# Kernel tuning notes

Hardware: AMD Instinct MI355X
Metric: run time of the kernel (lower is better)

Reference implementation:

```python
import jax, jax.numpy as jnp
import numpy as np
from itertools import permutations

M = 10          # number of masked tokens (logits.size(0) when whole_word=False)
VOCAB = 50257   # n_class


def setup_inputs() -> dict:
    key = jax.random.key(0)
    k1, k2 = jax.random.split(key)
    logits = jax.random.normal(k1, (M, VOCAB), dtype=jnp.float32)
    target = jax.random.randint(k2, (M,), 0, VOCAB, dtype=jnp.int64).astype(jnp.int32)
    # All M! permutations, enumerated exactly as itertools.permutations (lexicographic),
    # matching the torch module's iteration order (ties broken by first strict improvement).
    perms = jnp.asarray(np.array(list(permutations(range(M))), dtype=np.int32))
    return {"logits": logits, "target": target, "perms": perms}


def reference(logits, target, perms):
    # prob[i, v] = softmax over classes
    prob = jax.nn.softmax(logits, axis=-1)                      # [M, V]
    # S[i, j] = prob[i, target[j]]  (score of assigning slot j's target to position i)
    S = prob[:, target]                                         # [M, M]
    # score(p) = sum_i prob[i, target[p[i]]] = sum_i S[i, p[i]]
    rows = jnp.arange(S.shape[0], dtype=jnp.int32)[None, :]     # [1, M]
    scores = S[rows, perms].sum(axis=-1)                        # [P]
    # torch loop keeps the FIRST permutation achieving the max (strict > update);
    # jnp.argmax also returns the first occurrence of the max.
    best = jnp.argmax(scores)
    target_best = target[perms[best]]                           # [M]
    # CrossEntropyLoss(reduction='none') == -log_softmax gathered at target
    logp = jax.nn.log_softmax(logits, axis=-1)                  # [M, V]
    loss = -jnp.take_along_axis(logp, target_best[:, None].astype(jnp.int32), axis=1)[:, 0]
    return loss, target_best
```

## Files before the change

kernel.cpp:

```cpp
#include <hip/hip_runtime.h>

#define VOCAB 50257
#define M 10
#define NPERM 3628800
#define CHUNKS 32
#define CH 1571
#define NTHREADS_PERM 151200
#define PERM_BLOCKS 591

#define WS_PMAX 0
#define WS_PSUM 320
#define WS_RMAX 640
#define WS_RSUM 656
#define WS_S    672

__global__ __launch_bounds__(256) void chunkstats_kernel(
    const float* __restrict__ logits, float* __restrict__ ws) {
    const int r = blockIdx.x >> 5;
    const int c = blockIdx.x & 31;
    const int s = c * CH;
    const int e = (s + CH < VOCAB) ? s + CH : VOCAB;
    const float* __restrict__ x = logits + (size_t)r * VOCAB;
    const int tid = threadIdx.x;
    __shared__ float wred[4];

    float m = -3.4e38f;
    for (int j = s + tid; j < e; j += 256) m = fmaxf(m, x[j]);
    #pragma unroll
    for (int off = 32; off; off >>= 1) m = fmaxf(m, __shfl_down(m, off, 64));
    if ((tid & 63) == 0) wred[tid >> 6] = m;
    __syncthreads();
    const float cm = fmaxf(fmaxf(wred[0], wred[1]), fmaxf(wred[2], wred[3]));
    __syncthreads();

    float sum = 0.f;
    for (int j = s + tid; j < e; j += 256) sum += expf(x[j] - cm);
    #pragma unroll
    for (int off = 32; off; off >>= 1) sum += __shfl_down(sum, off, 64);
    if ((tid & 63) == 0) wred[tid >> 6] = sum;
    __syncthreads();
    if (tid == 0) {
        ws[WS_PMAX + blockIdx.x] = cm;
        ws[WS_PSUM + blockIdx.x] = wred[0] + wred[1] + wred[2] + wred[3];
    }
}

__global__ __launch_bounds__(320) void combine_kernel(
    const float* __restrict__ logits, const int* __restrict__ target,
    float* __restrict__ ws) {
    const int tid = threadIdx.x;
    const int r = tid >> 5;
    const float lm = ws[WS_PMAX + tid];
    float m = lm;
    #pragma unroll
    for (int off = 16; off; off >>= 1) m = fmaxf(m, __shfl_xor(m, off, 32));
    float contrib = ws[WS_PSUM + tid] * expf(lm - m);
    #pragma unroll
    for (int off = 16; off; off >>= 1) contrib += __shfl_xor(contrib, off, 32);
    if ((tid & 31) == 0) {
        ws[WS_RMAX + r] = m;
        ws[WS_RSUM + r] = contrib;
    }
    __syncthreads();
    if (tid < 100) {
        const int i = tid / 10;
        const int k = tid % 10;
        const int t = target[k];
        ws[WS_S + tid] =
            expf(logits[(size_t)i * VOCAB + t] - ws[WS_RMAX + i]) / ws[WS_RSUM + i];
    }
}

__global__ __launch_bounds__(256) void perm_kernel(
    const float* __restrict__ ws, unsigned long long* __restrict__ keys) {
    __shared__ float S[100];
    const int tid = threadIdx.x;
    if (tid < 100) S[tid] = ws[WS_S + tid];
    __syncthreads();

    const unsigned int t = blockIdx.x * 256u + tid;
    unsigned long long key = 0ull;
    if (t < NTHREADS_PERM) {
        const unsigned int base = t * 24u;
        unsigned int p = base;
        unsigned long long avail = 0x9876543210ull;
        float prefix = 0.f;
        const unsigned int fact6[6] = {362880u, 40320u, 5040u, 720u, 120u, 24u};
        #pragma unroll
        for (int pos = 0; pos < 6; ++pos) {
            const unsigned int f = fact6[pos];
            const unsigned int d = p / f;
            p -= d * f;
            const unsigned int sh = d * 4u;
            const unsigned int sym = (unsigned int)(avail >> sh) & 0xFu;
            avail = (avail & ((1ull << sh) - 1ull)) | ((avail >> (sh + 4u)) << sh);
            prefix += S[pos * 10 + sym];
        }
        const int q0 = (int)(avail & 0xF),        q1 = (int)((avail >> 4) & 0xF);
        const int q2 = (int)((avail >> 8) & 0xF), q3 = (int)((avail >> 12) & 0xF);
        const float s6[4] = {S[60+q0], S[60+q1], S[60+q2], S[60+q3]};
        const float s7[4] = {S[70+q0], S[70+q1], S[70+q2], S[70+q3]};
        const float s8[4] = {S[80+q0], S[80+q1], S[80+q2], S[80+q3]};
        const float s9[4] = {S[90+q0], S[90+q1], S[90+q2], S[90+q3]};
        constexpr unsigned char P[24][4] = {
            {0,1,2,3},{0,1,3,2},{0,2,1,3},{0,2,3,1},{0,3,1,2},{0,3,2,1},
            {1,0,2,3},{1,0,3,2},{1,2,0,3},{1,2,3,0},{1,3,0,2},{1,3,2,0},
            {2,0,1,3},{2,0,3,1},{2,1,0,3},{2,1,3,0},{2,3,0,1},{2,3,1,0},
            {3,0,1,2},{3,0,2,1},{3,1,0,2},{3,1,2,0},{3,2,0,1},{3,2,1,0}};
        float best = -1.f; unsigned int bl = 0;
        #pragma unroll
        for (int l = 0; l < 24; ++l) {
            const float sc =
                (((prefix + s6[P[l][0]]) + s7[P[l][1]]) + s8[P[l][2]]) + s9[P[l][3]];
            if (sc > best) { best = sc; bl = (unsigned int)l; }
        }
        const unsigned int gidx = base + bl;
        key = ((unsigned long long)__float_as_uint(best) << 32) |
              (unsigned long long)(0xFFFFFFFFu - gidx);
    }
    #pragma unroll
    for (int off = 32; off; off >>= 1) {
        const unsigned long long o = __shfl_down(key, off, 64);
        if (o > key) key = o;
    }
    __shared__ unsigned long long wk[4];
    if ((tid & 63) == 0) wk[tid >> 6] = key;
    __syncthreads();
    if (tid == 0) {
        unsigned long long k = wk[0];
        #pragma unroll
        for (int w = 1; w < 4; ++w) if (wk[w] > k) k = wk[w];
        keys[blockIdx.x] = k;
    }
}

__global__ __launch_bounds__(256) void final_kernel(
    const float* __restrict__ logits, const int* __restrict__ target,
    const float* __restrict__ ws, const unsigned long long* __restrict__ keys,
    float* __restrict__ out) {
    const int tid = threadIdx.x;
    unsigned long long k = 0ull;
    for (int i = tid; i < PERM_BLOCKS; i += 256) {
        const unsigned long long v = keys[i];
        if (v > k) k = v;
    }
    #pragma unroll
    for (int off = 32; off; off >>= 1) {
        const unsigned long long o = __shfl_down(k, off, 64);
        if (o > k) k = o;
    }
    __shared__ unsigned long long wk[4];
    __shared__ int perm[10];
    if ((tid & 63) == 0) wk[tid >> 6] = k;
    __syncthreads();
    if (tid == 0) {
        unsigned long long kk = wk[0];
        #pragma unroll
        for (int w = 1; w < 4; ++w) if (wk[w] > kk) kk = wk[w];
        unsigned int p = 0xFFFFFFFFu - (unsigned int)(kk & 0xFFFFFFFFull);
        unsigned long long avail = 0x9876543210ull;
        const unsigned int fact[9] = {362880u, 40320u, 5040u, 720u, 120u, 24u, 6u, 2u, 1u};
        #pragma unroll
        for (int pos = 0; pos < 9; ++pos) {
            const unsigned int f = fact[pos];
            const unsigned int d = p / f;
            p -= d * f;
            const unsigned int sh = d * 4u;
            perm[pos] = (int)((avail >> sh) & 0xFull);
            avail = (avail & ((1ull << sh) - 1ull)) | ((avail >> (sh + 4u)) << sh);
        }
        perm[9] = (int)(avail & 0xFull);
    }
    __syncthreads();
    if (tid < 10) {
        const int tb = target[perm[tid]];
        const float logp =
            logits[(size_t)tid * VOCAB + tb] - ws[WS_RMAX + tid] - logf(ws[WS_RSUM + tid]);
        out[tid]      = -logp;
        out[10 + tid] = (float)tb;
    }
}

extern "C" void kernel_launch(void* const* d_in, const int* in_sizes, int n_in,
                              void* d_out, int out_size, void* d_ws, size_t ws_size,
                              hipStream_t stream) {
    const float* logits = (const float*)d_in[0];
    const int*   target = (const int*)d_in[1];
    float* ws = (float*)d_ws;
    unsigned long long* keys = (unsigned long long*)((char*)d_ws + 4096);
    float* out = (float*)d_out;

    chunkstats_kernel<<<10 * CHUNKS, 256, 0, stream>>>(logits, ws);
    combine_kernel<<<1, 320, 0, stream>>>(logits, target, ws);
    perm_kernel<<<PERM_BLOCKS, 256, 0, stream>>>(ws, keys);
    final_kernel<<<1, 256, 0, stream>>>(logits, target, ws, keys, out);
}
```

Measured before the change: 18.20 us.

## Fuse combine, permutation search and final reduction into one last-block kernel

```diff
diff --git a/kernel.cpp b/kernel.cpp
--- a/kernel.cpp
+++ b/kernel.cpp
@@ -3,21 +3,20 @@
 #define VOCAB 50257
 #define M 10
 #define NPERM 3628800
-#define CHUNKS 32
-#define CH 1571
+#define CHUNKS 16
+#define CH 3142
 #define NTHREADS_PERM 151200
 #define PERM_BLOCKS 591
 
 #define WS_PMAX 0
-#define WS_PSUM 320
-#define WS_RMAX 640
-#define WS_RSUM 656
-#define WS_S    672
+#define WS_PSUM 160
 
 __global__ __launch_bounds__(256) void chunkstats_kernel(
-    const float* __restrict__ logits, float* __restrict__ ws) {
-    const int r = blockIdx.x >> 5;
-    const int c = blockIdx.x & 31;
+    const float* __restrict__ logits, float* __restrict__ ws,
+    unsigned int* __restrict__ counter) {
+    if (blockIdx.x == 0 && threadIdx.x == 0) *counter = 0u;
+    const int r = blockIdx.x >> 4;
+    const int c = blockIdx.x & 15;
     const int s = c * CH;
     const int e = (s + CH < VOCAB) ? s + CH : VOCAB;
     const float* __restrict__ x = logits + (size_t)r * VOCAB;
@@ -45,37 +44,31 @@
     }
 }
 
-__global__ __launch_bounds__(320) void combine_kernel(
+__global__ __launch_bounds__(256) void fused_perm_kernel(
     const float* __restrict__ logits, const int* __restrict__ target,
-    float* __restrict__ ws) {
+    const float* __restrict__ ws, unsigned long long* __restrict__ keys,
+    unsigned int* __restrict__ counter, float* __restrict__ out) {
+    __shared__ float S[100], rowmax[10], rowsum[10];
+    __shared__ unsigned long long wk[4];
+    __shared__ int perm[10];
+    __shared__ int isLast;
     const int tid = threadIdx.x;
-    const int r = tid >> 5;
-    const float lm = ws[WS_PMAX + tid];
-    float m = lm;
-    #pragma unroll
-    for (int off = 16; off; off >>= 1) m = fmaxf(m, __shfl_xor(m, off, 32));
-    float contrib = ws[WS_PSUM + tid] * expf(lm - m);
-    #pragma unroll
-    for (int off = 16; off; off >>= 1) contrib += __shfl_xor(contrib, off, 32);
-    if ((tid & 31) == 0) {
-        ws[WS_RMAX + r] = m;
-        ws[WS_RSUM + r] = contrib;
+
+    if (tid < 160) {
+        const float lm = ws[WS_PMAX + tid];
+        float m = lm;
+        #pragma unroll
+        for (int off = 8; off; off >>= 1) m = fmaxf(m, __shfl_xor(m, off, 16));
+        float c = ws[WS_PSUM + tid] * expf(lm - m);
+        #pragma unroll
+        for (int off = 8; off; off >>= 1) c += __shfl_xor(c, off, 16);
+        if ((tid & 15) == 0) { rowmax[tid >> 4] = m; rowsum[tid >> 4] = c; }
     }
     __syncthreads();
     if (tid < 100) {
-        const int i = tid / 10;
-        const int k = tid % 10;
-        const int t = target[k];
-        ws[WS_S + tid] =
-            expf(logits[(size_t)i * VOCAB + t] - ws[WS_RMAX + i]) / ws[WS_RSUM + i];
+        const int i = tid / 10, k = tid % 10;
+        S[tid] = expf(logits[(size_t)i * VOCAB + target[k]] - rowmax[i]) / rowsum[i];
     }
-}
-
-__global__ __launch_bounds__(256) void perm_kernel(
-    const float* __restrict__ ws, unsigned long long* __restrict__ keys) {
-    __shared__ float S[100];
-    const int tid = threadIdx.x;
-    if (tid < 100) S[tid] = ws[WS_S + tid];
     __syncthreads();
 
     const unsigned int t = blockIdx.x * 256u + tid;
@@ -123,7 +116,6 @@
         const unsigned long long o = __shfl_down(key, off, 64);
         if (o > key) key = o;
     }
-    __shared__ unsigned long long wk[4];
     if ((tid & 63) == 0) wk[tid >> 6] = key;
     __syncthreads();
     if (tid == 0) {
@@ -131,14 +123,14 @@
         #pragma unroll
         for (int w = 1; w < 4; ++w) if (wk[w] > k) k = wk[w];
         keys[blockIdx.x] = k;
+        __threadfence();
+        const unsigned int prev = atomicAdd(counter, 1u);
+        isLast = (prev == PERM_BLOCKS - 1) ? 1 : 0;
     }
-}
+    __syncthreads();
+    if (!isLast) return;
+    __threadfence();
 
-__global__ __launch_bounds__(256) void final_kernel(
-    const float* __restrict__ logits, const int* __restrict__ target,
-    const float* __restrict__ ws, const unsigned long long* __restrict__ keys,
-    float* __restrict__ out) {
-    const int tid = threadIdx.x;
     unsigned long long k = 0ull;
     for (int i = tid; i < PERM_BLOCKS; i += 256) {
         const unsigned long long v = keys[i];
@@ -149,8 +141,6 @@
         const unsigned long long o = __shfl_down(k, off, 64);
         if (o > k) k = o;
     }
-    __shared__ unsigned long long wk[4];
-    __shared__ int perm[10];
     if ((tid & 63) == 0) wk[tid >> 6] = k;
     __syncthreads();
     if (tid == 0) {
@@ -175,7 +165,7 @@
     if (tid < 10) {
         const int tb = target[perm[tid]];
         const float logp =
-            logits[(size_t)tid * VOCAB + tb] - ws[WS_RMAX + tid] - logf(ws[WS_RSUM + tid]);
+            logits[(size_t)tid * VOCAB + tb] - rowmax[tid] - logf(rowsum[tid]);
         out[tid]      = -logp;
         out[10 + tid] = (float)tb;
     }
@@ -187,11 +177,11 @@
     const float* logits = (const float*)d_in[0];
     const int*   target = (const int*)d_in[1];
     float* ws = (float*)d_ws;
+    unsigned int* counter = (unsigned int*)((char*)d_ws + 2048);
     unsigned long long* keys = (unsigned long long*)((char*)d_ws + 4096);
     float* out = (float*)d_out;
 
-    chunkstats_kernel<<<10 * CHUNKS, 256, 0, stream>>>(logits, ws);
-    combine_kernel<<<1, 320, 0, stream>>>(logits, target, ws);
-    perm_kernel<<<PERM_BLOCKS, 256, 0, stream>>>(ws, keys);
-    final_kernel<<<1, 256, 0, stream>>>(logits, target, ws, keys, out);
+    chunkstats_kernel<<<10 * CHUNKS, 256, 0, stream>>>(logits, ws, counter);
+    fused_perm_kernel<<<PERM_BLOCKS, 256, 0, stream>>>(logits, target, ws, keys,
+                                                       counter, out);
 }
```

Measured after the change: 26.38 us. 44.9% more time.
